# Optimization experiments

Hardware: AMD Instinct MI355X
Metric: run time of the kernel (lower is better)

## Reference

```python
import jax, jax.numpy as jnp
import numpy as np

GRAPH_SIZE = 512  # N: graph_size from init


def setup_inputs() -> dict:
    key = jax.random.key(0)
    k1, k2 = jax.random.split(key)
    B, N, C_IN, C_OUT = 128, GRAPH_SIZE, 128, 128
    # X packs [adjacency | features] along last dim, matching the torch forward
    X = jax.random.uniform(k1, (B, N, N + C_IN), dtype=jnp.float32)
    W = jax.random.normal(k2, (C_IN, C_OUT), dtype=jnp.float32)
    return {"X": X, "W": W}


def reference(X, W):
    N = GRAPH_SIZE
    A = X[:, :, :N]            # [B, N, N] dense adjacency
    feat = X[:, :, N:]         # [B, N, C_in]
    # D = diag(rowsum(A)); pinv(D).sqrt() == diag(1/sqrt(deg)) with 0 where deg==0
    deg = jnp.sum(A, axis=2)   # [B, N]
    d_inv_sqrt = jnp.where(deg > 0, 1.0 / jnp.sqrt(deg), 0.0)
    A_hat = A + jnp.eye(N, dtype=A.dtype)  # A + I
    # D^-1/2 @ A_hat @ D^-1/2 as elementwise row/col scaling (diag matmuls)
    A_norm = d_inv_sqrt[:, :, None] * A_hat * d_inv_sqrt[:, None, :]
    # relu(A_norm @ X @ W)
    h = jnp.einsum('bnm,bmf->bnf', A_norm, feat)
    out = jax.nn.relu(jnp.einsum('bnf,fo->bno', h, W))
    return jnp.concatenate([A, out], axis=2)  # [B, N, N + C_out]
```

## Files before the change

kernel.cpp:

```cpp
#include <hip/hip_runtime.h>
#include <stdint.h>

#define GS   512
#define CF   128
#define XROW 640
#define NB   128

typedef __attribute__((ext_vector_type(4))) float          f32x4;
typedef __attribute__((ext_vector_type(8))) short          s16x8;
typedef __attribute__((ext_vector_type(4))) unsigned short u16x4;
typedef __attribute__((ext_vector_type(8))) unsigned short u16x8;

__device__ __forceinline__ unsigned short f2bf(float f) {
    unsigned u = __builtin_bit_cast(unsigned, f);
    u = (u + 0x7fffu + ((u >> 16) & 1u)) >> 16;
    return (unsigned short)u;
}
__device__ __forceinline__ float bf2f(unsigned short h) {
    unsigned u = ((unsigned)h) << 16;
    return __builtin_bit_cast(float, u);
}
__device__ __forceinline__ void glds16(const void* g, void* l) {
    __builtin_amdgcn_global_load_lds(
        (const __attribute__((address_space(1))) void*)g,
        (__attribute__((address_space(3))) void*)l, 16, 0, 0);
}

__global__ __launch_bounds__(256) void k0_wt(const float* __restrict__ W,
                                             unsigned short* __restrict__ WTst) {
    const int e = blockIdx.x * 256 + threadIdx.x;
    const int j = e & 7, f = (e >> 3) & 127, q = e >> 10;
    const int c = (q >> 2) * 32 + (q & 3) * 8 + j;
    WTst[e] = f2bf(W[c * CF + f]);
}

__global__ __launch_bounds__(256) void k12(const float* __restrict__ X,
                                           const unsigned short* __restrict__ WTst,
                                           float* __restrict__ out,
                                           float* __restrict__ dis,
                                           unsigned short* __restrict__ Abf,
                                           unsigned short* __restrict__ fwdT) {
    __shared__ __align__(16) unsigned short sfb[64 * 128];
    __shared__ __align__(16) unsigned short swt[16384];
    __shared__ __align__(16) float sdis[64];
    const int t = threadIdx.x, l = t & 63, wv = t >> 6;
    const int m0 = blockIdx.x << 6;
    const int b = m0 >> 9, ml0 = m0 & (GS - 1);

#pragma unroll
    for (int it = 0; it < 8; ++it)
        glds16((const char*)WTst + it * 4096 + wv * 1024 + l * 16,
               (char*)swt + it * 4096 + wv * 1024);

    for (int p = 0; p < 16; ++p) {
        const int rw = (p << 2) + wv;
        const int gr = m0 + rw;
        const f32x4* rp = (const f32x4*)(X + (size_t)gr * XROW);
        f32x4 v0 = rp[2 * l], v1 = rp[2 * l + 1];
        f32x4 vf;
        if (l < 32) vf = rp[128 + l];
        f32x4* op = (f32x4*)(out + (size_t)gr * XROW);
        op[2 * l] = v0; op[2 * l + 1] = v1;
        u16x8 o;
        o[0] = f2bf(v0[0]); o[1] = f2bf(v0[1]); o[2] = f2bf(v0[2]); o[3] = f2bf(v0[3]);
        o[4] = f2bf(v1[0]); o[5] = f2bf(v1[1]); o[6] = f2bf(v1[2]); o[7] = f2bf(v1[3]);
        *(u16x8*)((char*)Abf + ((size_t)gr << 10) + (l << 4)) = o;
        if (l < 32) {
            u16x4 fo;
            fo[0] = f2bf(vf[0]); fo[1] = f2bf(vf[1]); fo[2] = f2bf(vf[2]); fo[3] = f2bf(vf[3]);
            int ad = (rw << 8) + (l << 3);
            ad ^= (rw & 7) << 4;
            *(u16x4*)((char*)sfb + ad) = fo;
        }
        float s = (v0[0] + v0[1]) + (v0[2] + v0[3]) + (v1[0] + v1[1]) + (v1[2] + v1[3]);
#pragma unroll
        for (int off = 32; off; off >>= 1) s += __shfl_xor(s, off, 64);
        if (l == 0) {
            float d = (s > 0.f) ? (1.f / sqrtf(s)) : 0.f;
            sdis[rw] = d; dis[gr] = d;
        }
    }
    __syncthreads();

    const int wr = wv >> 1, wc = wv & 1, lr = l & 15, lk = l >> 4;
    f32x4 acc[2][4];
#pragma unroll
    for (int i = 0; i < 2; ++i)
#pragma unroll
        for (int j = 0; j < 4; ++j)
#pragma unroll
            for (int r = 0; r < 4; ++r) acc[i][j][r] = 0.f;

#pragma unroll
    for (int ks = 0; ks < 4; ++ks) {
        s16x8 af[2];
#pragma unroll
        for (int i = 0; i < 2; ++i) {
            int row = (wr << 5) + (i << 4) + lr;
            int ad = (row << 8) + (((ks << 2) | lk) << 4);
            ad ^= (row & 7) << 4;
            af[i] = *(const s16x8*)((char*)sfb + ad);
        }
#pragma unroll
        for (int j = 0; j < 4; ++j) {
            int f = (wc << 6) + (j << 4) + lr;
            s16x8 bfr = *(const s16x8*)&swt[((((ks << 2) | lk) << 7) | f) << 3];
#pragma unroll
            for (int i = 0; i < 2; ++i)
                acc[i][j] = __builtin_amdgcn_mfma_f32_16x16x32_bf16(af[i], bfr, acc[i][j], 0, 0, 0);
        }
    }

#pragma unroll
    for (int i = 0; i < 2; ++i) {
        int mr = (wr << 5) + (i << 4) + (lk << 2);
        f32x4 d4 = *(const f32x4*)&sdis[mr];
        int mg = ml0 + mr;
        int ktm = mg >> 5, q3 = (mg >> 3) & 3, jm = mg & 7;
#pragma unroll
        for (int j = 0; j < 4; ++j) {
            int f = (wc << 6) + (j << 4) + lr;
            u16x4 o;
            o[0] = f2bf(d4[0] * acc[i][j][0]);
            o[1] = f2bf(d4[1] * acc[i][j][1]);
            o[2] = f2bf(d4[2] * acc[i][j][2]);
            o[3] = f2bf(d4[3] * acc[i][j][3]);
            *(u16x4*)((char*)fwdT + ((size_t)b << 17) + (((ktm << 2) | q3) << 11)
                      + (f << 4) + (jm << 1)) = o;
        }
    }
}

__global__ __launch_bounds__(256) void k3_gcn(const unsigned short* __restrict__ Abf,
                                              const float* __restrict__ dis,
                                              const unsigned short* __restrict__ fwdT,
                                              float* __restrict__ out) {
    __shared__ __align__(16) unsigned short sb[2][8192];
    const int t = threadIdx.x, l = t & 63, wv = t >> 6, lr = l & 15, lk = l >> 4;
    const int b = blockIdx.x >> 3, bm0 = (blockIdx.x & 7) << 6;
    const char* Bt = (const char*)fwdT + ((size_t)b << 17);
    const char* Ab = (const char*)Abf
        + (((size_t)(b * GS + bm0 + (wv << 4) + lr)) << 10) + (lk << 4);

    auto stage = [&](int buf, int ph) {
#pragma unroll
        for (int it = 0; it < 4; ++it)
            glds16(Bt + (ph << 14) + it * 4096 + wv * 1024 + l * 16,
                   (char*)sb[buf] + it * 4096 + wv * 1024);
    };

    f32x4 acc[8];
#pragma unroll
    for (int j = 0; j < 8; ++j)
#pragma unroll
        for (int r = 0; r < 4; ++r) acc[j][r] = 0.f;

    stage(0, 0);
    s16x8 a0 = *(const s16x8*)(Ab);
    s16x8 a1 = *(const s16x8*)(Ab + 64);
    int cur = 0;
    for (int ph = 0; ph < 8; ++ph) {
        __syncthreads();
        if (ph < 7) stage(cur ^ 1, ph + 1);
        s16x8 n0 = a0, n1 = a1;
        if (ph < 7) {
            n0 = *(const s16x8*)(Ab + ((2 * ph + 2) << 6));
            n1 = *(const s16x8*)(Ab + ((2 * ph + 3) << 6));
        }
#pragma unroll
        for (int j = 0; j < 8; ++j) {
            s16x8 bfr = *(const s16x8*)&sb[cur][(lk << 10) + (j << 7) + (lr << 3)];
            acc[j] = __builtin_amdgcn_mfma_f32_16x16x32_bf16(a0, bfr, acc[j], 0, 0, 0);
        }
#pragma unroll
        for (int j = 0; j < 8; ++j) {
            s16x8 bfr = *(const s16x8*)&sb[cur][4096 + (lk << 10) + (j << 7) + (lr << 3)];
            acc[j] = __builtin_amdgcn_mfma_f32_16x16x32_bf16(a1, bfr, acc[j], 0, 0, 0);
        }
        a0 = n0; a1 = n1; cur ^= 1;
    }

    const int n0r = bm0 + (wv << 4) + (lk << 2);
    f32x4 d4 = *(const f32x4*)&dis[(b << 9) + n0r];
    const int ktm = n0r >> 5, q3 = (n0r >> 3) & 3, jm = n0r & 7;
#pragma unroll
    for (int j = 0; j < 8; ++j) {
        int f = (j << 4) + lr;
        u16x4 fw = *(const u16x4*)(Bt + (((ktm << 2) | q3) << 11) + (f << 4) + (jm << 1));
        float* ob = out + ((size_t)(b * GS + n0r)) * XROW + GS + f;
#pragma unroll
        for (int r = 0; r < 4; ++r) {
            float v = d4[r] * (acc[j][r] + bf2f(fw[r]));
            ob[(size_t)r * XROW] = v > 0.f ? v : 0.f;
        }
    }
}

extern "C" void kernel_launch(void* const* d_in, const int* in_sizes, int n_in,
                              void* d_out, int out_size, void* d_ws, size_t ws_size,
                              hipStream_t stream) {
    const float* X = (const float*)d_in[0];
    const float* W = (const float*)d_in[1];
    float* out = (float*)d_out;
    float*          dis  = (float*)d_ws;
    unsigned short* WTst = (unsigned short*)((char*)d_ws + 262144);
    unsigned short* fwdT = (unsigned short*)((char*)d_ws + 294912);
    unsigned short* Abf  = (unsigned short*)((char*)d_ws + 17072128);

    hipLaunchKernelGGL(k0_wt, dim3(64),            dim3(256), 0, stream, W, WTst);
    hipLaunchKernelGGL(k12,   dim3(NB * GS / 64),  dim3(256), 0, stream, X, WTst, out, dis, Abf, fwdT);
    hipLaunchKernelGGL(k3_gcn, dim3(NB * GS / 64), dim3(256), 0, stream, Abf, dis, fwdT, out);
}
```

Measured before the change: 340.2 us.

## Drop W LDS staging in k12, spread feature loads, remap k3 block order

In k12 the 32KB LDS copy of the transposed weights is removed and B fragments are read straight from global/L2, and the kernel now declares a minimum occupancy of 4 blocks per SM. Feature loads are spread across all 64 lanes as float2 instead of half the lanes loading float4. The row-sum reduction is split into a partial shuffle followed by an LDS-based finish. k3's block index is permuted so consecutive blocks come from different batches. Together these cut LDS use to raise occupancy and change L2 access locality, at the cost of more global traffic for W fragments.

```diff
diff --git a/kernel.cpp b/kernel.cpp
--- a/kernel.cpp
+++ b/kernel.cpp
@@ -7,6 +7,7 @@
 #define NB   128
 
 typedef __attribute__((ext_vector_type(4))) float          f32x4;
+typedef __attribute__((ext_vector_type(2))) float          f32x2;
 typedef __attribute__((ext_vector_type(8))) short          s16x8;
 typedef __attribute__((ext_vector_type(4))) unsigned short u16x4;
 typedef __attribute__((ext_vector_type(8))) unsigned short u16x8;
@@ -34,50 +35,52 @@
     WTst[e] = f2bf(W[c * CF + f]);
 }
 
-__global__ __launch_bounds__(256) void k12(const float* __restrict__ X,
-                                           const unsigned short* __restrict__ WTst,
-                                           float* __restrict__ out,
-                                           float* __restrict__ dis,
-                                           unsigned short* __restrict__ Abf,
-                                           unsigned short* __restrict__ fwdT) {
+__global__ __launch_bounds__(256, 4) void k12(const float* __restrict__ X,
+                                              const unsigned short* __restrict__ WTst,
+                                              float* __restrict__ out,
+                                              float* __restrict__ dis,
+                                              unsigned short* __restrict__ Abf,
+                                              unsigned short* __restrict__ fwdT) {
     __shared__ __align__(16) unsigned short sfb[64 * 128];
-    __shared__ __align__(16) unsigned short swt[16384];
+    __shared__ __align__(16) float spart[64 * 16];
     __shared__ __align__(16) float sdis[64];
     const int t = threadIdx.x, l = t & 63, wv = t >> 6;
     const int m0 = blockIdx.x << 6;
     const int b = m0 >> 9, ml0 = m0 & (GS - 1);
 
-#pragma unroll
-    for (int it = 0; it < 8; ++it)
-        glds16((const char*)WTst + it * 4096 + wv * 1024 + l * 16,
-               (char*)swt + it * 4096 + wv * 1024);
-
     for (int p = 0; p < 16; ++p) {
         const int rw = (p << 2) + wv;
         const int gr = m0 + rw;
-        const f32x4* rp = (const f32x4*)(X + (size_t)gr * XROW);
+        const float* row = X + (size_t)gr * XROW;
+        const f32x4* rp = (const f32x4*)row;
         f32x4 v0 = rp[2 * l], v1 = rp[2 * l + 1];
-        f32x4 vf;
-        if (l < 32) vf = rp[128 + l];
+        f32x2 vf = *(const f32x2*)(row + GS + 2 * l);
         f32x4* op = (f32x4*)(out + (size_t)gr * XROW);
         op[2 * l] = v0; op[2 * l + 1] = v1;
         u16x8 o;
         o[0] = f2bf(v0[0]); o[1] = f2bf(v0[1]); o[2] = f2bf(v0[2]); o[3] = f2bf(v0[3]);
         o[4] = f2bf(v1[0]); o[5] = f2bf(v1[1]); o[6] = f2bf(v1[2]); o[7] = f2bf(v1[3]);
         *(u16x8*)((char*)Abf + ((size_t)gr << 10) + (l << 4)) = o;
-        if (l < 32) {
-            u16x4 fo;
-            fo[0] = f2bf(vf[0]); fo[1] = f2bf(vf[1]); fo[2] = f2bf(vf[2]); fo[3] = f2bf(vf[3]);
-            int ad = (rw << 8) + (l << 3);
-            ad ^= (rw & 7) << 4;
-            *(u16x4*)((char*)sfb + ad) = fo;
-        }
+        unsigned fo = (unsigned)f2bf(vf[0]) | ((unsigned)f2bf(vf[1]) << 16);
+        int ad = (rw << 8) + (l << 2);
+        ad ^= (rw & 7) << 4;
+        *(unsigned*)((char*)sfb + ad) = fo;
         float s = (v0[0] + v0[1]) + (v0[2] + v0[3]) + (v1[0] + v1[1]) + (v1[2] + v1[3]);
-#pragma unroll
-        for (int off = 32; off; off >>= 1) s += __shfl_xor(s, off, 64);
-        if (l == 0) {
+        s += __shfl_xor(s, 32);
+        s += __shfl_xor(s, 16);
+        if (l < 16) spart[(rw << 4) + l] = s;
+    }
+    __syncthreads();
+
+    {
+        const int r = t >> 2, c = t & 3;
+        f32x4 pv = *(const f32x4*)&spart[(r << 4) + (c << 2)];
+        float s = (pv[0] + pv[1]) + (pv[2] + pv[3]);
+        s += __shfl_xor(s, 1);
+        s += __shfl_xor(s, 2);
+        if (c == 0) {
             float d = (s > 0.f) ? (1.f / sqrtf(s)) : 0.f;
-            sdis[rw] = d; dis[gr] = d;
+            sdis[r] = d; dis[m0 + r] = d;
         }
     }
     __syncthreads();
@@ -104,7 +107,7 @@
 #pragma unroll
         for (int j = 0; j < 4; ++j) {
             int f = (wc << 6) + (j << 4) + lr;
-            s16x8 bfr = *(const s16x8*)&swt[((((ks << 2) | lk) << 7) | f) << 3];
+            s16x8 bfr = *(const s16x8*)(WTst + (((((ks << 2) | lk) << 7) | f) << 3));
 #pragma unroll
             for (int i = 0; i < 2; ++i)
                 acc[i][j] = __builtin_amdgcn_mfma_f32_16x16x32_bf16(af[i], bfr, acc[i][j], 0, 0, 0);
@@ -137,7 +140,9 @@
                                               float* __restrict__ out) {
     __shared__ __align__(16) unsigned short sb[2][8192];
     const int t = threadIdx.x, l = t & 63, wv = t >> 6, lr = l & 15, lk = l >> 4;
-    const int b = blockIdx.x >> 3, bm0 = (blockIdx.x & 7) << 6;
+    const int ord = blockIdx.x;
+    const int L = ((ord & 7) << 7) + (ord >> 3);
+    const int b = L >> 3, bm0 = (L & 7) << 6;
     const char* Bt = (const char*)fwdT + ((size_t)b << 17);
     const char* Ab = (const char*)Abf
         + (((size_t)(b * GS + bm0 + (wv << 4) + lr)) << 10) + (lk << 4);
```

Measured after the change: 335.4 us. About the same (-1.4%).
